# Kernel tuning notes

Measured on AMD Instinct MI355X. Metric: run time of the kernel, lower is better.

Reference implementation:

```python
import jax, jax.numpy as jnp
import numpy as np

B, S, L, H, D = 32, 512, 8, 1024, 64  # batch, max seq len, max span, hidden, MLP width


def setup_inputs() -> dict:
    key = jax.random.key(0)
    ks = jax.random.split(key, 8)
    return {
        "hidden": jax.random.normal(ks[0], (B, S, H), jnp.float32),
        "seq_lengths": jax.random.randint(ks[1], (B,), S // 2, S + 1),
        "term_weight": jax.random.normal(ks[2], (H,), jnp.float32),
        "W1": jax.random.normal(ks[3], (H, D), jnp.float32) * 0.02,
        "b1": jnp.zeros((D,), jnp.float32),
        "W2": jax.random.normal(ks[4], (D, 1), jnp.float32) * 0.02,
        "b2": jnp.zeros((1,), jnp.float32),
        "Ws": jax.random.normal(ks[5], (H, 1), jnp.float32) * 0.02,
        "bs": jnp.zeros((1,), jnp.float32),
    }


def reference(hidden, seq_lengths, term_weight, W1, b1, W2, b2, Ws, bs):
    """Batched candidate-span TermAttention + span scoring.

    For each sentence b (true length seq_lengths[b]) and start s, spans of
    nominal length l+1 (l in 0..L-1) cover positions s..s+l clipped to the
    sentence end, exactly as get_candidate_span_pairs/get_span_hiddens.
    TermAttention: softmax over MLP((h * w)) within the span, weighted sum,
    then spanEmb2Score linear -> scalar per span.
    """
    Bn, Sn, Hn = hidden.shape
    j = jnp.arange(L)
    s = jnp.arange(Sn)
    pos = jnp.minimum(s[:, None] + j[None, :], Sn - 1)          # [S,L] clipped gather idx
    g = hidden[:, pos]                                           # [B,S,L,H] span positions
    # per-position attention logit (independent of span length)
    e = (jax.nn.relu((g * term_weight) @ W1 + b1) @ W2 + b2)[..., 0]  # [B,S,L]
    # valid_pos[b,s,jp]: position s+jp is inside sentence b
    valid_pos = (s[:, None] + j[None, :])[None] < seq_lengths[:, None, None]  # [B,S,L]
    # m[b,s,l,jp]: position jp belongs to span of length l+1 and is in-sentence
    tri = j[:, None] >= j[None, :]                               # [L,L] jp <= l
    m = valid_pos[:, :, None, :] & tri[None, None]               # [B,S,L,L]
    logits = jnp.where(m, e[:, :, None, :], -1e9)
    a = jax.nn.softmax(logits, axis=-1) * m                      # [B,S,L,L]
    emb = jnp.einsum('bslj,bsjh->bslh', a, g)                    # span embeddings
    scores = (emb @ Ws + bs)[..., 0]                             # [B,S,L]
    valid_span = s[None, :, None] < seq_lengths[:, None, None]
    return jnp.where(valid_span, scores, 0.0)
```

## Files before the change

kernel.cpp:

```cpp
#include <hip/hip_runtime.h>
#include <hip/hip_bf16.h>

#define BB 32
#define SS 512
#define LL 8
#define HH 1024
#define DD 64

#define BM 64
#define ROWSTR 1032

typedef __attribute__((ext_vector_type(8))) short bf16x8;
typedef __attribute__((ext_vector_type(8))) unsigned short u16x8;
typedef __attribute__((ext_vector_type(4))) float f32x4;

__device__ __forceinline__ unsigned short f2bf(float x) {
    unsigned int u = __float_as_uint(x);
    u += 0x7FFFu + ((u >> 16) & 1u);
    return (unsigned short)(u >> 16);
}

__global__ __launch_bounds__(256) void k_prep(const float* __restrict__ W1,
                                              const float* __restrict__ tw,
                                              unsigned short* __restrict__ Bpack) {
    int g = blockIdx.x * 256 + threadIdx.x;
    int ln = g & 63;
    int c  = (g >> 6) & 31;
    int cg = g >> 11;
    int n  = cg * 16 + (ln & 15);
    int hb = (ln >> 4) * 8 + c * 32;
    u16x8 pk;
#pragma unroll
    for (int j = 0; j < 8; j++) {
        float val = tw[hb + j] * W1[(hb + j) * DD + n];
        pk[j] = f2bf(val);
    }
    *(u16x8*)(Bpack + (size_t)g * 8) = pk;
}

__global__ __launch_bounds__(1024, 1) void k_main(
        const float* __restrict__ hidden,
        const unsigned short* __restrict__ Bpack,
        const float* __restrict__ b1,
        const float* __restrict__ W2,
        const float* __restrict__ b2,
        const float* __restrict__ Ws,
        float* __restrict__ e1,
        float* __restrict__ vout) {
    __shared__ unsigned short Alds[BM * ROWSTR];
    __shared__ float eplds[4][BM];

    const int tid = threadIdx.x;
    const int row0 = blockIdx.x * BM;

    {
        const int r  = tid >> 4;
        const int co = (tid & 15) * 4;
        const float* arow = hidden + (size_t)(row0 + r) * HH + co;
        float4 h[16];
#pragma unroll
        for (int i = 0; i < 16; i++) h[i] = *(const float4*)(arow + i * 64);

        float vp = 0.f;
#pragma unroll
        for (int i = 0; i < 16; i++) {
            float4 w4 = *(const float4*)(Ws + co + i * 64);
            vp += h[i].x * w4.x + h[i].y * w4.y + h[i].z * w4.z + h[i].w * w4.w;
            ushort4 a4;
            a4.x = f2bf(h[i].x); a4.y = f2bf(h[i].y);
            a4.z = f2bf(h[i].z); a4.w = f2bf(h[i].w);
            *(ushort4*)&Alds[r * ROWSTR + co + i * 64] = a4;
        }
        vp += __shfl_xor(vp, 1);
        vp += __shfl_xor(vp, 2);
        vp += __shfl_xor(vp, 4);
        vp += __shfl_xor(vp, 8);
        if ((tid & 15) == 0) vout[row0 + r] = vp;
    }
    __syncthreads();

    const int wv   = tid >> 6;
    const int rg   = wv >> 2;
    const int cg   = wv & 3;
    const int ln   = tid & 63;
    const int ln15 = ln & 15;
    const int quad = ln >> 4;

    const unsigned short* bptr = Bpack + ((size_t)(cg * 32) * 64 + ln) * 8;
    const unsigned short* aptr = &Alds[(rg * 16 + ln15) * ROWSTR + quad * 8];

    bf16x8 bf[4];
#pragma unroll
    for (int i = 0; i < 4; i++) bf[i] = *(const bf16x8*)(bptr + i * 512);

    f32x4 acc = {0.f, 0.f, 0.f, 0.f};
#pragma unroll
    for (int c = 0; c < 32; c++) {
        bf16x8 bcur = bf[c & 3];
        if (c + 4 < 32) bf[c & 3] = *(const bf16x8*)(bptr + (c + 4) * 512);
        bf16x8 afrag = *(const bf16x8*)(aptr + c * 32);
        acc = __builtin_amdgcn_mfma_f32_16x16x32_bf16(afrag, bcur, acc, 0, 0, 0);
    }

    const int col = cg * 16 + ln15;
    const float b1c = b1[col];
    const float w2c = W2[col];
    float ep[4];
#pragma unroll
    for (int reg = 0; reg < 4; reg++) {
        ep[reg] = fmaxf(acc[reg] + b1c, 0.f) * w2c;
    }
#pragma unroll
    for (int off = 1; off < 16; off <<= 1) {
#pragma unroll
        for (int i = 0; i < 4; i++) ep[i] += __shfl_xor(ep[i], off);
    }
    if (ln15 == 0) {
#pragma unroll
        for (int reg = 0; reg < 4; reg++)
            eplds[cg][rg * 16 + quad * 4 + reg] = ep[reg];
    }
    __syncthreads();
    if (tid < BM) {
        e1[row0 + tid] = b2[0] + eplds[0][tid] + eplds[1][tid] + eplds[2][tid] + eplds[3][tid];
    }
}

__global__ __launch_bounds__(256) void k_span(
        const float* __restrict__ e1,
        const float* __restrict__ v,
        const int* __restrict__ seq_lengths,
        const float* __restrict__ bs,
        float* __restrict__ out) {
    int i = blockIdx.x * 256 + threadIdx.x;
    int b = i >> 9;
    int s = i & (SS - 1);
    int sl = seq_lengths[b];
    float res[LL];

    if (s >= sl) {
#pragma unroll
        for (int l = 0; l < LL; l++) res[l] = 0.f;
    } else {
        const float bsv = bs[0];
        float e[LL], vv[LL];
        int base = b << 9;
#pragma unroll
        for (int j = 0; j < LL; j++) {
            int pos = s + j; if (pos > SS - 1) pos = SS - 1;
            e[j]  = e1[base + pos];
            vv[j] = v[base + pos];
        }
        float M = e[0], Z = 1.f, W = vv[0];
        res[0] = W / Z + bsv;
#pragma unroll
        for (int l = 1; l < LL; l++) {
            if (s + l < sl) {
                float el = e[l];
                if (el > M) {
                    float c = __expf(M - el);
                    Z = Z * c + 1.f;
                    W = W * c + vv[l];
                    M = el;
                } else {
                    float p = __expf(el - M);
                    Z += p;
                    W += p * vv[l];
                }
            }
            res[l] = W / Z + bsv;
        }
    }
    float4* o = (float4*)(out + (size_t)i * LL);
    o[0] = make_float4(res[0], res[1], res[2], res[3]);
    o[1] = make_float4(res[4], res[5], res[6], res[7]);
}

extern "C" void kernel_launch(void* const* d_in, const int* in_sizes, int n_in,
                              void* d_out, int out_size, void* d_ws, size_t ws_size,
                              hipStream_t stream) {
    const float* hidden = (const float*)d_in[0];
    const int*   seqlen = (const int*)d_in[1];
    const float* tw     = (const float*)d_in[2];
    const float* W1     = (const float*)d_in[3];
    const float* b1     = (const float*)d_in[4];
    const float* W2     = (const float*)d_in[5];
    const float* b2     = (const float*)d_in[6];
    const float* Ws     = (const float*)d_in[7];
    const float* bs     = (const float*)d_in[8];
    float* out = (float*)d_out;

    unsigned short* Bpack = (unsigned short*)d_ws;
    float* e1 = (float*)((char*)d_ws + 131072);
    float* vv = (float*)((char*)d_ws + 131072 + 65536);

    k_prep<<<32, 256, 0, stream>>>(W1, tw, Bpack);

    k_main<<<(BB * SS) / BM, 1024, 0, stream>>>(hidden, Bpack, b1, W2, b2, Ws, e1, vv);

    k_span<<<(BB * SS) / 256, 256, 0, stream>>>(e1, vv, seqlen, bs, out);
}
```

Before: 114.9 us.

## Split K across waves and feed MFMA directly from global loads

The main kernel now uses 16-row blocks of 256 threads. Each wave owns a quarter of the hidden dimension and converts fp32 hidden values straight into bf16 MFMA fragments in registers, with no LDS staging of the whole row tile. Partial accumulators for all 64 output columns are reduced across waves through a small LDS buffer before the ReLU/W2 epilogue. This removes the large LDS tile and its occupancy limit and gives more blocks, so memory latency can be hidden better. The cost is an extra cross-wave reduction, and each block reloads the B fragments from global or cache.

```diff
diff --git a/kernel.cpp b/kernel.cpp
--- a/kernel.cpp
+++ b/kernel.cpp
@@ -6,9 +6,6 @@
 #define LL 8
 #define HH 1024
 #define DD 64
-
-#define BM 64
-#define ROWSTR 1032
 
 typedef __attribute__((ext_vector_type(8))) short bf16x8;
 typedef __attribute__((ext_vector_type(8))) unsigned short u16x8;
@@ -38,7 +35,7 @@
     *(u16x8*)(Bpack + (size_t)g * 8) = pk;
 }
 
-__global__ __launch_bounds__(1024, 1) void k_main(
+__global__ __launch_bounds__(256, 4) void k_main(
         const float* __restrict__ hidden,
         const unsigned short* __restrict__ Bpack,
         const float* __restrict__ b1,
@@ -47,82 +44,74 @@
         const float* __restrict__ Ws,
         float* __restrict__ e1,
         float* __restrict__ vout) {
-    __shared__ unsigned short Alds[BM * ROWSTR];
-    __shared__ float eplds[4][BM];
+    __shared__ float red[4][16][65];
+    __shared__ float vred[4][16];
 
-    const int tid = threadIdx.x;
-    const int row0 = blockIdx.x * BM;
+    const int tid  = threadIdx.x;
+    const int wv   = tid >> 6;
+    const int ln   = tid & 63;
+    const int ln15 = ln & 15;
+    const int quad = ln >> 4;
+    const int row0 = blockIdx.x * 16;
 
-    {
-        const int r  = tid >> 4;
-        const int co = (tid & 15) * 4;
-        const float* arow = hidden + (size_t)(row0 + r) * HH + co;
-        float4 h[16];
+    const float* aptr = hidden + (size_t)(row0 + ln15) * HH + wv * 256 + quad * 8;
+    const float* wsp  = Ws + wv * 256 + quad * 8;
+    const unsigned short* bptr = Bpack + ((size_t)(wv * 8) * 64 + ln) * 8;
+
+    f32x4 acc[4];
 #pragma unroll
-        for (int i = 0; i < 16; i++) h[i] = *(const float4*)(arow + i * 64);
+    for (int cg = 0; cg < 4; cg++) acc[cg] = (f32x4){0.f, 0.f, 0.f, 0.f};
+    float vp = 0.f;
 
-        float vp = 0.f;
 #pragma unroll
-        for (int i = 0; i < 16; i++) {
-            float4 w4 = *(const float4*)(Ws + co + i * 64);
-            vp += h[i].x * w4.x + h[i].y * w4.y + h[i].z * w4.z + h[i].w * w4.w;
-            ushort4 a4;
-            a4.x = f2bf(h[i].x); a4.y = f2bf(h[i].y);
-            a4.z = f2bf(h[i].z); a4.w = f2bf(h[i].w);
-            *(ushort4*)&Alds[r * ROWSTR + co + i * 64] = a4;
+    for (int cc = 0; cc < 8; cc++) {
+        float4 h0 = *(const float4*)(aptr + cc * 32);
+        float4 h1 = *(const float4*)(aptr + cc * 32 + 4);
+        float4 w0 = *(const float4*)(wsp + cc * 32);
+        float4 w1 = *(const float4*)(wsp + cc * 32 + 4);
+        vp += h0.x * w0.x + h0.y * w0.y + h0.z * w0.z + h0.w * w0.w
+            + h1.x * w1.x + h1.y * w1.y + h1.z * w1.z + h1.w * w1.w;
+        bf16x8 af;
+        af[0] = (short)f2bf(h0.x); af[1] = (short)f2bf(h0.y);
+        af[2] = (short)f2bf(h0.z); af[3] = (short)f2bf(h0.w);
+        af[4] = (short)f2bf(h1.x); af[5] = (short)f2bf(h1.y);
+        af[6] = (short)f2bf(h1.z); af[7] = (short)f2bf(h1.w);
+#pragma unroll
+        for (int cg = 0; cg < 4; cg++) {
+            bf16x8 bfrag = *(const bf16x8*)(bptr + (cg * 32 + cc) * 512);
+            acc[cg] = __builtin_amdgcn_mfma_f32_16x16x32_bf16(af, bfrag, acc[cg], 0, 0, 0);
         }
-        vp += __shfl_xor(vp, 1);
-        vp += __shfl_xor(vp, 2);
-        vp += __shfl_xor(vp, 4);
-        vp += __shfl_xor(vp, 8);
-        if ((tid & 15) == 0) vout[row0 + r] = vp;
+    }
+
+    vp += __shfl_xor(vp, 16);
+    vp += __shfl_xor(vp, 32);
+    if (quad == 0) vred[wv][ln15] = vp;
+
+#pragma unroll
+    for (int cg = 0; cg < 4; cg++) {
+#pragma unroll
+        for (int reg = 0; reg < 4; reg++) {
+            red[wv][quad * 4 + reg][cg * 16 + ln15] = acc[cg][reg];
+        }
     }
     __syncthreads();
 
-    const int wv   = tid >> 6;
-    const int rg   = wv >> 2;
-    const int cg   = wv & 3;
-    const int ln   = tid & 63;
-    const int ln15 = ln & 15;
-    const int quad = ln >> 4;
-
-    const unsigned short* bptr = Bpack + ((size_t)(cg * 32) * 64 + ln) * 8;
-    const unsigned short* aptr = &Alds[(rg * 16 + ln15) * ROWSTR + quad * 8];
-
-    bf16x8 bf[4];
+    {
+        const int rl = tid >> 4;
+        const int c0 = (tid & 15) * 4;
+        float ep = 0.f;
 #pragma unroll
-    for (int i = 0; i < 4; i++) bf[i] = *(const bf16x8*)(bptr + i * 512);
-
-    f32x4 acc = {0.f, 0.f, 0.f, 0.f};
-#pragma unroll
-    for (int c = 0; c < 32; c++) {
-        bf16x8 bcur = bf[c & 3];
-        if (c + 4 < 32) bf[c & 3] = *(const bf16x8*)(bptr + (c + 4) * 512);
-        bf16x8 afrag = *(const bf16x8*)(aptr + c * 32);
-        acc = __builtin_amdgcn_mfma_f32_16x16x32_bf16(afrag, bcur, acc, 0, 0, 0);
-    }
-
-    const int col = cg * 16 + ln15;
-    const float b1c = b1[col];
-    const float w2c = W2[col];
-    float ep[4];
-#pragma unroll
-    for (int reg = 0; reg < 4; reg++) {
-        ep[reg] = fmaxf(acc[reg] + b1c, 0.f) * w2c;
-    }
-#pragma unroll
-    for (int off = 1; off < 16; off <<= 1) {
-#pragma unroll
-        for (int i = 0; i < 4; i++) ep[i] += __shfl_xor(ep[i], off);
-    }
-    if (ln15 == 0) {
-#pragma unroll
-        for (int reg = 0; reg < 4; reg++)
-            eplds[cg][rg * 16 + quad * 4 + reg] = ep[reg];
-    }
-    __syncthreads();
-    if (tid < BM) {
-        e1[row0 + tid] = b2[0] + eplds[0][tid] + eplds[1][tid] + eplds[2][tid] + eplds[3][tid];
+        for (int j = 0; j < 4; j++) {
+            int c = c0 + j;
+            float x = red[0][rl][c] + red[1][rl][c] + red[2][rl][c] + red[3][rl][c];
+            ep += fmaxf(x + b1[c], 0.f) * W2[c];
+        }
+        ep += __shfl_xor(ep, 1);
+        ep += __shfl_xor(ep, 2);
+        ep += __shfl_xor(ep, 4);
+        ep += __shfl_xor(ep, 8);
+        if ((tid & 15) == 0) e1[row0 + rl] = ep + b2[0];
+        if (tid < 16) vout[row0 + tid] = vred[0][tid] + vred[1][tid] + vred[2][tid] + vred[3][tid];
     }
 }
 
@@ -196,7 +185,7 @@
 
     k_prep<<<32, 256, 0, stream>>>(W1, tw, Bpack);
 
-    k_main<<<(BB * SS) / BM, 1024, 0, stream>>>(hidden, Bpack, b1, W2, b2, Ws, e1, vv);
+    k_main<<<(BB * SS) / 16, 256, 0, stream>>>(hidden, Bpack, b1, W2, b2, Ws, e1, vv);
 
     k_span<<<(BB * SS) / 256, 256, 0, stream>>>(e1, vv, seqlen, bs, out);
 }
```

Result: slower. 120.2 us (+4.6%).
